# Optimization experiments

Measured on AMD Instinct MI355X. Metric: run time of the kernel, lower is better.

Reference implementation:

```python
import jax, jax.numpy as jnp
import numpy as np

B, N, D = 32, 540, 512
H = 8
DH = D // H
MAX_LEN = 540
POS_CLIP = MAX_LEN - 1


def setup_inputs() -> dict:
    key = jax.random.key(0)
    ks = jax.random.split(key, 12)
    s = 0.02
    inp = {
        "query": jax.random.normal(ks[0], (B, N, D), dtype=jnp.float32),
        "Wq": jax.random.normal(ks[1], (D, D), dtype=jnp.float32) * s,
        "bq": jnp.zeros((D,), jnp.float32),
        "Wk": jax.random.normal(ks[2], (D, D), dtype=jnp.float32) * s,
        "bk": jnp.zeros((D,), jnp.float32),
        "Wv": jax.random.normal(ks[3], (D, D), dtype=jnp.float32) * s,
        "bv": jnp.zeros((D,), jnp.float32),
        "Wh": jax.random.normal(ks[4], (D, D), dtype=jnp.float32) * s,
        "bh": jnp.zeros((D,), jnp.float32),
        "pos_k": jax.random.uniform(ks[5], (2 * POS_CLIP + 1, DH), dtype=jnp.float32, minval=-0.05, maxval=0.05),
        "gamma": jnp.ones((D,), jnp.float32),
        "beta": jnp.zeros((D,), jnp.float32),
        "valid_len": jax.random.randint(ks[6], (B,), 1, N + 1, dtype=jnp.int32),
    }
    return inp


def _split_heads(x):
    # [B, N, D] -> [H*B, N, DH], head-major on axis 0 (matches tf.concat(tf.split(x,H,-1),0))
    return x.reshape(B, N, H, DH).transpose(2, 0, 1, 3).reshape(H * B, N, DH)


def reference(query, Wq, bq, Wk, bk, Wv, bv, Wh, bh, pos_k, gamma, beta, valid_len):
    q = _split_heads(query @ Wq + bq)  # [HB, N, DH]
    k = _split_heads(query @ Wk + bk)
    v = _split_heads(query @ Wv + bv)

    QK = jnp.einsum("xqd,xkd->xqk", q, k)  # [HB, N, N]

    # relative position bias (Shaw et al. 2018)
    rel = jnp.arange(N)[None, :] - jnp.arange(N)[:, None]
    rel = jnp.clip(rel, -POS_CLIP, POS_CLIP) + POS_CLIP
    pos_enc_k = pos_k[rel]  # [N, N, DH]
    QR = jnp.einsum("xqd,qkd->xqk", q, pos_enc_k)

    attn = (QK + QR) / jnp.sqrt(jnp.float32(DH))

    # key-side sequence mask, broadcast over heads and query rows
    key_mask = jnp.arange(N)[None, :] < valid_len[:, None]  # [B, N]
    key_mask = jnp.tile(key_mask[:, None, :], (H, N, 1))  # [HB, N, N]
    attn = jnp.where(key_mask, attn, jnp.float32(-1e12))
    attn = jax.nn.softmax(attn, axis=-1)

    out = jnp.einsum("xqk,xkd->xqd", attn, v)  # [HB, N, DH]
    out = out.reshape(H, B, N, DH).transpose(1, 2, 0, 3).reshape(B, N, D)
    out = out @ Wh + bh
    out = out + query

    # layer norm over last axis
    mean = jnp.mean(out, axis=-1, keepdims=True)
    var = jnp.mean(jnp.square(out - mean), axis=-1, keepdims=True)
    normalized = (out - mean) * jax.lax.rsqrt(var + 1e-7)
    return gamma * normalized + beta
```

## Files before the change

### kernel.cpp

```cpp
#include <hip/hip_runtime.h>
#include <hip/hip_bf16.h>

typedef __hip_bfloat16 bf16;

#define NB 32
#define NSEQ 540
#define ND 512
#define NH 8
#define NDH 64
#define NHB 256
#define NM 17280
#define NPOS 1079
#define VTP 544

typedef __bf16 v8bf __attribute__((ext_vector_type(8)));
typedef float f32x4 __attribute__((ext_vector_type(4)));

union U8 {
  uint4 u;
  unsigned short s[8];
  v8bf v;
};

__device__ __forceinline__ unsigned short f2b(float x) {
  union { float f; unsigned u; } c;
  c.f = x;
  const unsigned r = c.u + 0x7fffu + ((c.u >> 16) & 1u);
  return (unsigned short)(r >> 16);
}

__device__ __forceinline__ float b2f16(unsigned short s) {
  return __uint_as_float(((unsigned)s) << 16);
}

__device__ __forceinline__ void cvt16(const float* __restrict__ p,
                                      unsigned short* __restrict__ dst) {
  unsigned short s[16];
#pragma unroll
  for (int i = 0; i < 4; i++) {
    const float4 v = *(const float4*)(p + i * 4);
    s[i * 4 + 0] = f2b(v.x);
    s[i * 4 + 1] = f2b(v.y);
    s[i * 4 + 2] = f2b(v.z);
    s[i * 4 + 3] = f2b(v.w);
  }
  *(uint4*)dst = *(uint4*)s;
  *(uint4*)(dst + 8) = *(uint4*)(s + 8);
}

__global__ __launch_bounds__(256) void pos_cvt(const float* __restrict__ pos,
                                              unsigned short* __restrict__ posb) {
  const int i = blockIdx.x * 256 + threadIdx.x;
  if (i < NPOS * NDH) posb[i] = f2b(pos[i]);
}

__global__ __launch_bounds__(256) void wcvt(
    const float* __restrict__ Wq, const float* __restrict__ Wk,
    const float* __restrict__ Wv, const float* __restrict__ Wh,
    unsigned short* __restrict__ Wt) {
  __shared__ unsigned short T[64][72];
  const int tid = threadIdx.x;
  const int sel = blockIdx.z;
  const float* W = (sel == 0) ? Wq : (sel == 1) ? Wk : (sel == 2) ? Wv : Wh;
  unsigned short* out = Wt + (size_t)sel * ND * ND;
  const int k0 = blockIdx.x * 64, n0 = blockIdx.y * 64;
  const int r = tid >> 2, g = tid & 3;
  cvt16(W + (size_t)(k0 + r) * ND + n0 + g * 16, &T[r][g * 16]);
  __syncthreads();
  unsigned short s[16];
#pragma unroll
  for (int j = 0; j < 16; j++) s[j] = T[g * 16 + j][r];
  unsigned short* dst = out + (size_t)(n0 + r) * ND + k0 + g * 16;
  *(uint4*)dst = *(uint4*)s;
  *(uint4*)(dst + 8) = *(uint4*)(s + 8);
}

#define GEMM_CORE(APTR)                                                           \
  for (int k0 = 0; k0 < 512; k0 += 32) {                                          \
    __syncthreads();                                                              \
    cvt16(APTR + (size_t)(m0 + srow) * ND + k0 + sh, &As[srow][sh]);              \
    {                                                                             \
      const unsigned short* bp = Bt + (size_t)(n0 + srow) * ND + k0 + sh;         \
      *(uint4*)&Bs[srow][sh] = *(const uint4*)bp;                                 \
      *(uint4*)&Bs[srow][sh + 8] = *(const uint4*)(bp + 8);                       \
    }                                                                             \
    __syncthreads();                                                              \
    U8 af[4], bfr[4];                                                             \
    _Pragma("unroll")                                                             \
    for (int mi = 0; mi < 4; mi++)                                                \
      af[mi].u = *(const uint4*)&As[wr * 64 + mi * 16 + l15][quad * 8];           \
    _Pragma("unroll")                                                             \
    for (int ni = 0; ni < 4; ni++)                                                \
      bfr[ni].u = *(const uint4*)&Bs[wc * 64 + ni * 16 + l15][quad * 8];          \
    _Pragma("unroll")                                                             \
    for (int mi = 0; mi < 4; mi++)                                                \
      _Pragma("unroll")                                                           \
      for (int ni = 0; ni < 4; ni++)                                              \
        acc[mi][ni] = __builtin_amdgcn_mfma_f32_16x16x32_bf16(                    \
            af[mi].v, bfr[ni].v, acc[mi][ni], 0, 0, 0);                           \
  }

__global__ __launch_bounds__(256, 2) void qkv_mfma(
    const float* __restrict__ X, const unsigned short* __restrict__ Wt,
    const float* __restrict__ bq, const float* __restrict__ bk,
    const float* __restrict__ bv,
    bf16* __restrict__ qh, bf16* __restrict__ kh, bf16* __restrict__ vt) {
  __shared__ unsigned short As[128][40];
  __shared__ unsigned short Bs[128][40];
  const int tid = threadIdx.x;
  const int sel = blockIdx.z;
  const unsigned short* Bt = Wt + (size_t)sel * ND * ND;
  const float* bias = (sel == 0) ? bq : (sel == 1) ? bk : bv;
  const int m0 = blockIdx.y * 128, n0 = blockIdx.x * 128;
  const int lane = tid & 63, w = tid >> 6;
  const int wr = w & 1, wc = w >> 1;
  const int l15 = lane & 15, quad = lane >> 4;
  const int srow = tid >> 1, sh = (tid & 1) * 16;

  f32x4 acc[4][4];
#pragma unroll
  for (int mi = 0; mi < 4; mi++)
#pragma unroll
    for (int ni = 0; ni < 4; ni++) acc[mi][ni] = (f32x4){0.f, 0.f, 0.f, 0.f};

  GEMM_CORE(X)

  if (sel != 2) {
    unsigned short* o = (unsigned short*)((sel == 0) ? qh : kh);
#pragma unroll
    for (int mi = 0; mi < 4; mi++) {
      const int m = m0 + wr * 64 + mi * 16 + quad * 4;
      const int bidx = m / NSEQ;
      const int seq0 = m - bidx * NSEQ;
#pragma unroll
      for (int ni = 0; ni < 4; ni++) {
        const int n = n0 + wc * 64 + ni * 16 + l15;
        const int h = n >> 6, dh = n & 63;
        const float bsv = bias[n];
        const size_t base = (((size_t)(h * NB + bidx)) * NSEQ + seq0) * NDH + dh;
#pragma unroll
        for (int i = 0; i < 4; i++)
          o[base + (size_t)i * NDH] = f2b(acc[mi][ni][i] + bsv);
      }
    }
  } else {
    unsigned short* o = (unsigned short*)vt;
#pragma unroll
    for (int mi = 0; mi < 4; mi++) {
      const int m = m0 + wr * 64 + mi * 16 + quad * 4;
      const int bidx = m / NSEQ;
      const int seq0 = m - bidx * NSEQ;
#pragma unroll
      for (int ni = 0; ni < 4; ni++) {
        const int n = n0 + wc * 64 + ni * 16 + l15;
        const int h = n >> 6, dh = n & 63;
        const float bsv = bias[n];
        unsigned short pk[4];
#pragma unroll
        for (int i = 0; i < 4; i++) pk[i] = f2b(acc[mi][ni][i] + bsv);
        *(uint2*)(o + (((size_t)(h * NB + bidx)) * NDH + dh) * VTP + seq0) =
            *(uint2*)pk;
      }
    }
  }
}

__global__ __launch_bounds__(256, 2) void out_mfma(
    const float* __restrict__ ctx, const unsigned short* __restrict__ Wht,
    const float* __restrict__ bh, const float* __restrict__ query,
    float* __restrict__ tmp) {
  __shared__ unsigned short As[128][40];
  __shared__ unsigned short Bs[128][40];
  const int tid = threadIdx.x;
  const unsigned short* Bt = Wht;
  const int m0 = blockIdx.y * 128, n0 = blockIdx.x * 128;
  const int lane = tid & 63, w = tid >> 6;
  const int wr = w & 1, wc = w >> 1;
  const int l15 = lane & 15, quad = lane >> 4;
  const int srow = tid >> 1, sh = (tid & 1) * 16;

  f32x4 acc[4][4];
#pragma unroll
  for (int mi = 0; mi < 4; mi++)
#pragma unroll
    for (int ni = 0; ni < 4; ni++) acc[mi][ni] = (f32x4){0.f, 0.f, 0.f, 0.f};

  GEMM_CORE(ctx)

#pragma unroll
  for (int mi = 0; mi < 4; mi++) {
    const int m = m0 + wr * 64 + mi * 16 + quad * 4;
#pragma unroll
    for (int ni = 0; ni < 4; ni++) {
      const int n = n0 + wc * 64 + ni * 16 + l15;
      const float bsv = bh[n];
#pragma unroll
      for (int i = 0; i < 4; i++) {
        const size_t off = (size_t)(m + i) * ND + n;
        tmp[off] = acc[mi][ni][i] + bsv + query[off];
      }
    }
  }
}

#define PW 584

__global__ __launch_bounds__(256, 5) void attn(
    const bf16* __restrict__ qh, const bf16* __restrict__ kh,
    const bf16* __restrict__ vt, const unsigned short* __restrict__ posb,
    const int* __restrict__ vlen, float* __restrict__ ctx) {
  __shared__ unsigned short P[16][PW];
  __shared__ float Tt[2][16][84];
  __shared__ float red4[16][4];
  __shared__ float sinv[16];

  const int tid = threadIdx.x;
  const int lane = tid & 63;
  const int w = tid >> 6;
  const int l15 = lane & 15;
  const int quad = lane >> 4;
  const int qb = blockIdx.x;
  const int x = blockIdx.y;
  const int b = x & 31, h = x >> 5;
  const int q0 = qb * 16;
  const int valid = vlen[b];
  const int NT = (valid + 63) >> 6;
  const int NC = (valid + 31) >> 5;
  const bf16* qbase = qh + (size_t)x * NSEQ * NDH;
  const unsigned short* kbase = (const unsigned short*)(kh + (size_t)x * NSEQ * NDH);
  const unsigned short* vbase = (const unsigned short*)(vt + (size_t)x * NDH * VTP);

  U8 aq0, aq1;
  {
    const int q = q0 + l15;
    if (q < NSEQ) {
      aq0.u = *(const uint4*)(qbase + (size_t)q * NDH + quad * 8);
      aq1.u = *(const uint4*)(qbase + (size_t)q * NDH + 32 + quad * 8);
    } else {
      aq0.u = make_uint4(0, 0, 0, 0);
      aq1.u = make_uint4(0, 0, 0, 0);
    }
  }

  U8 ck0, ck1, cp0, cp1, ce0, ce1;
  {
    const int key = w * 16 + l15;
    ck0.u = *(const uint4*)(kbase + (size_t)key * NDH + quad * 8);
    ck1.u = *(const uint4*)(kbase + (size_t)key * NDH + 32 + quad * 8);
    const long pr = (long)(524 - q0 + w * 16 + l15);
    cp0.u = *(const uint4*)(posb + pr * NDH + quad * 8);
    cp1.u = *(const uint4*)(posb + pr * NDH + 32 + quad * 8);
    if (w == 0) {
      const long pr2 = (long)(524 - q0 + 64 + l15);
      ce0.u = *(const uint4*)(posb + pr2 * NDH + quad * 8);
      ce1.u = *(const uint4*)(posb + pr2 * NDH + 32 + quad * 8);
    }
  }

  float pmax[4];
#pragma unroll
  for (int i = 0; i < 4; i++) pmax[i] = -1e30f;

  for (int kt = 0; kt < NT; kt++) {
    const int buf = kt & 1;
    U8 nk0, nk1, np0, np1, ne0, ne1;
    if (kt < NT - 1) {
      const int k1 = kt * 64 + 64;
      const int key = k1 + w * 16 + l15;
      nk0.u = *(const uint4*)(kbase + (size_t)key * NDH + quad * 8);
      nk1.u = *(const uint4*)(kbase + (size_t)key * NDH + 32 + quad * 8);
      const long pr = (long)(k1 - q0 + 524 + w * 16 + l15);
      np0.u = *(const uint4*)(posb + pr * NDH + quad * 8);
      np1.u = *(const uint4*)(posb + pr * NDH + 32 + quad * 8);
      if (w == 0) {
        const long pr2 = (long)(k1 - q0 + 524 + 64 + l15);
        ne0.u = *(const uint4*)(posb + pr2 * NDH + quad * 8);
        ne1.u = *(const uint4*)(posb + pr2 * NDH + 32 + quad * 8);
      }
    }

    f32x4 accqk = {0.f, 0.f, 0.f, 0.f};
    accqk = __builtin_amdgcn_mfma_f32_16x16x32_bf16(aq0.v, ck0.v, accqk, 0, 0, 0);
    accqk = __builtin_amdgcn_mfma_f32_16x16x32_bf16(aq1.v, ck1.v, accqk, 0, 0, 0);
    {
      f32x4 accT = {0.f, 0.f, 0.f, 0.f};
      accT = __builtin_amdgcn_mfma_f32_16x16x32_bf16(aq0.v, cp0.v, accT, 0, 0, 0);
      accT = __builtin_amdgcn_mfma_f32_16x16x32_bf16(aq1.v, cp1.v, accT, 0, 0, 0);
#pragma unroll
      for (int i = 0; i < 4; i++) Tt[buf][quad * 4 + i][w * 16 + l15] = accT[i];
      if (w == 0) {
        f32x4 accT2 = {0.f, 0.f, 0.f, 0.f};
        accT2 = __builtin_amdgcn_mfma_f32_16x16x32_bf16(aq0.v, ce0.v, accT2, 0, 0, 0);
        accT2 = __builtin_amdgcn_mfma_f32_16x16x32_bf16(aq1.v, ce1.v, accT2, 0, 0, 0);
#pragma unroll
        for (int i = 0; i < 4; i++) Tt[buf][quad * 4 + i][64 + l15] = accT2[i];
      }
    }
    __syncthreads();
    {
      const int k0 = kt * 64;
      const int kk = w * 16 + l15;
      const bool cm = (k0 + kk) < valid;
#pragma unroll
      for (int i = 0; i < 4; i++) {
        const int qq = quad * 4 + i;
        const float v = (accqk[i] + Tt[buf][qq][kk + 15 - qq]) * 0.125f;
        P[qq][k0 + kk] = f2b(v);
        if (cm) pmax[i] = fmaxf(pmax[i], v);
      }
    }
    ck0 = nk0; ck1 = nk1; cp0 = np0; cp1 = np1;
    if (w == 0) { ce0 = ne0; ce1 = ne1; }
  }

#pragma unroll
  for (int m = 1; m < 16; m <<= 1) {
#pragma unroll
    for (int i = 0; i < 4; i++)
      pmax[i] = fmaxf(pmax[i], __shfl_xor(pmax[i], m, 16));
  }
  if (l15 == 0) {
#pragma unroll
    for (int i = 0; i < 4; i++) red4[quad * 4 + i][w] = pmax[i];
  }

  const int dh = w * 16 + l15;
  const unsigned short* vrow = vbase + (size_t)dh * VTP;
  U8 cv;
  cv.u = *(const uint4*)(vrow + quad * 8);

  __syncthreads();

  {
    const int r = tid >> 4, c = tid & 15;
    const float4 rm = *(const float4*)red4[r];
    const float rowmax = fmaxf(fmaxf(rm.x, rm.y), fmaxf(rm.z, rm.w));
    const int nv = (valid + 7) >> 3;
    float sl = 0.f;
    for (int ch = c; ch < nv; ch += 16) {
      const uint4 u = *(const uint4*)&P[r][ch * 8];
      unsigned ue[4];
#pragma unroll
      for (int jj = 0; jj < 4; jj++) {
        const unsigned uu = ((const unsigned*)&u)[jj];
        const float lo = __uint_as_float(uu << 16);
        const float hi = __uint_as_float(uu & 0xffff0000u);
        float el = __expf(lo - rowmax);
        float eh = __expf(hi - rowmax);
        const int cb = ch * 8 + jj * 2;
        el = (cb < valid) ? el : 0.f;
        eh = (cb + 1 < valid) ? eh : 0.f;
        sl += el + eh;
        ue[jj] = (unsigned)f2b(el) | ((unsigned)f2b(eh) << 16);
      }
      *(uint4*)&P[r][ch * 8] = *(const uint4*)ue;
    }
    for (int ch = c; ch < 72; ch += 16) {
      if (ch >= nv) *(uint4*)&P[r][ch * 8] = make_uint4(0, 0, 0, 0);
    }
#pragma unroll
    for (int m = 1; m < 16; m <<= 1) sl += __shfl_xor(sl, m, 16);
    if (c == 0) sinv[r] = 1.f / sl;
  }
  __syncthreads();

  f32x4 acco = {0.f, 0.f, 0.f, 0.f};
  for (int ci = 0; ci < NC; ci++) {
    U8 nv_;
    if (ci + 1 < NC) nv_.u = *(const uint4*)(vrow + (ci + 1) * 32 + quad * 8);
    U8 ap;
    ap.u = *(const uint4*)&P[l15][ci * 32 + quad * 8];
    acco = __builtin_amdgcn_mfma_f32_16x16x32_bf16(ap.v, cv.v, acco, 0, 0, 0);
    cv = nv_;
  }
#pragma unroll
  for (int i = 0; i < 4; i++) {
    const int q = q0 + quad * 4 + i;
    if (q < NSEQ) {
      ctx[((size_t)b * NSEQ + q) * ND + h * NDH + dh] = acco[i] * sinv[quad * 4 + i];
    }
  }
}

__global__ __launch_bounds__(256) void lnorm(
    const float* __restrict__ tmp, const float* __restrict__ gamma,
    const float* __restrict__ beta, float* __restrict__ out) {
  __shared__ float sred[256];
  const int row = blockIdx.x;
  const int tid = threadIdx.x;
  const size_t base = (size_t)row * 512;
  const float x0 = tmp[base + tid];
  const float x1 = tmp[base + 256 + tid];

  sred[tid] = x0 + x1;
  __syncthreads();
  for (int o = 128; o > 0; o >>= 1) {
    if (tid < o) sred[tid] += sred[tid + o];
    __syncthreads();
  }
  const float mean = sred[0] * (1.f / 512.f);
  __syncthreads();
  const float d0 = x0 - mean, d1 = x1 - mean;
  sred[tid] = d0 * d0 + d1 * d1;
  __syncthreads();
  for (int o = 128; o > 0; o >>= 1) {
    if (tid < o) sred[tid] += sred[tid + o];
    __syncthreads();
  }
  const float var = sred[0] * (1.f / 512.f);
  const float rstd = rsqrtf(var + 1e-7f);
  out[base + tid] = d0 * rstd * gamma[tid] + beta[tid];
  out[base + 256 + tid] = d1 * rstd * gamma[tid + 256] + beta[tid + 256];
}

extern "C" void kernel_launch(void* const* d_in, const int* in_sizes, int n_in,
                              void* d_out, int out_size, void* d_ws, size_t ws_size,
                              hipStream_t stream) {
  const float* query = (const float*)d_in[0];
  const float* Wq = (const float*)d_in[1];
  const float* bq = (const float*)d_in[2];
  const float* Wk = (const float*)d_in[3];
  const float* bk = (const float*)d_in[4];
  const float* Wv = (const float*)d_in[5];
  const float* bv = (const float*)d_in[6];
  const float* Wh = (const float*)d_in[7];
  const float* bh = (const float*)d_in[8];
  const float* pos = (const float*)d_in[9];
  const float* gamma = (const float*)d_in[10];
  const float* beta = (const float*)d_in[11];
  const int* vlen = (const int*)d_in[12];

  bf16* ws = (bf16*)d_ws;
  const size_t QSZ = (size_t)NHB * NSEQ * NDH;
  const size_t VSZ = (size_t)NHB * NDH * VTP;
  bf16* qh = ws;
  bf16* kh = ws + QSZ;
  bf16* vt = ws + 2 * QSZ;
  unsigned short* posb = (unsigned short*)(ws + 2 * QSZ + VSZ);
  unsigned short* Wtb = posb + (size_t)NPOS * NDH;
  float* ctx = (float*)d_out;
  float* tmp = (float*)d_ws;
  (void)ws_size;

  pos_cvt<<<dim3(270), 256, 0, stream>>>(pos, posb);
  wcvt<<<dim3(8, 8, 4), 256, 0, stream>>>(Wq, Wk, Wv, Wh, Wtb);
  qkv_mfma<<<dim3(4, 135, 3), 256, 0, stream>>>(query, Wtb, bq, bk, bv, qh, kh, vt);
  attn<<<dim3(34, 256), 256, 0, stream>>>(qh, kh, vt, posb, vlen, ctx);
  out_mfma<<<dim3(4, 135), 256, 0, stream>>>(ctx, Wtb + 3 * (size_t)ND * ND, bh, query, tmp);
  lnorm<<<NM, 256, 0, stream>>>(tmp, gamma, beta, (float*)d_out);
}
```

Baseline: 345.5 us.

## Replace shared-memory relative-position skew with per-wave shuffles, drop block barrier

The attention loop used to write each wave's Q·pos MFMA tile into a shared buffer, sync the block, and read back diagonally skewed values. Now each wave computes two adjacent 16-row position tiles itself and builds the skew with cross-lane shuffles. This removes the shared-memory round trip and one __syncthreads per key tile, at the cost of doubling the position MFMAs and position loads per wave. The launch-bounds occupancy hint for both GEMM kernels also rises from 2 to 3 blocks per SIMD, which may limit registers.

```diff
diff --git a/kernel.cpp b/kernel.cpp
--- a/kernel.cpp
+++ b/kernel.cpp
@@ -100,7 +100,7 @@
             af[mi].v, bfr[ni].v, acc[mi][ni], 0, 0, 0);                           \
   }
 
-__global__ __launch_bounds__(256, 2) void qkv_mfma(
+__global__ __launch_bounds__(256, 3) void qkv_mfma(
     const float* __restrict__ X, const unsigned short* __restrict__ Wt,
     const float* __restrict__ bq, const float* __restrict__ bk,
     const float* __restrict__ bv,
@@ -165,7 +165,7 @@
   }
 }
 
-__global__ __launch_bounds__(256, 2) void out_mfma(
+__global__ __launch_bounds__(256, 3) void out_mfma(
     const float* __restrict__ ctx, const unsigned short* __restrict__ Wht,
     const float* __restrict__ bh, const float* __restrict__ query,
     float* __restrict__ tmp) {
@@ -210,7 +210,6 @@
     const bf16* __restrict__ vt, const unsigned short* __restrict__ posb,
     const int* __restrict__ vlen, float* __restrict__ ctx) {
   __shared__ unsigned short P[16][PW];
-  __shared__ float Tt[2][16][84];
   __shared__ float red4[16][4];
   __shared__ float sinv[16];
 
@@ -242,7 +241,7 @@
     }
   }
 
-  U8 ck0, ck1, cp0, cp1, ce0, ce1;
+  U8 ck0, ck1, cp0, cp1, cq0, cq1;
   {
     const int key = w * 16 + l15;
     ck0.u = *(const uint4*)(kbase + (size_t)key * NDH + quad * 8);
@@ -250,11 +249,8 @@
     const long pr = (long)(524 - q0 + w * 16 + l15);
     cp0.u = *(const uint4*)(posb + pr * NDH + quad * 8);
     cp1.u = *(const uint4*)(posb + pr * NDH + 32 + quad * 8);
-    if (w == 0) {
-      const long pr2 = (long)(524 - q0 + 64 + l15);
-      ce0.u = *(const uint4*)(posb + pr2 * NDH + quad * 8);
-      ce1.u = *(const uint4*)(posb + pr2 * NDH + 32 + quad * 8);
-    }
+    cq0.u = *(const uint4*)(posb + (pr + 16) * NDH + quad * 8);
+    cq1.u = *(const uint4*)(posb + (pr + 16) * NDH + 32 + quad * 8);
   }
 
   float pmax[4];
@@ -262,8 +258,7 @@
   for (int i = 0; i < 4; i++) pmax[i] = -1e30f;
 
   for (int kt = 0; kt < NT; kt++) {
-    const int buf = kt & 1;
-    U8 nk0, nk1, np0, np1, ne0, ne1;
+    U8 nk0, nk1, np0, np1, nq0, nq1;
     if (kt < NT - 1) {
       const int k1 = kt * 64 + 64;
       const int key = k1 + w * 16 + l15;
@@ -272,31 +267,20 @@
       const long pr = (long)(k1 - q0 + 524 + w * 16 + l15);
       np0.u = *(const uint4*)(posb + pr * NDH + quad * 8);
       np1.u = *(const uint4*)(posb + pr * NDH + 32 + quad * 8);
-      if (w == 0) {
-        const long pr2 = (long)(k1 - q0 + 524 + 64 + l15);
-        ne0.u = *(const uint4*)(posb + pr2 * NDH + quad * 8);
-        ne1.u = *(const uint4*)(posb + pr2 * NDH + 32 + quad * 8);
-      }
+      nq0.u = *(const uint4*)(posb + (pr + 16) * NDH + quad * 8);
+      nq1.u = *(const uint4*)(posb + (pr + 16) * NDH + 32 + quad * 8);
     }
 
     f32x4 accqk = {0.f, 0.f, 0.f, 0.f};
     accqk = __builtin_amdgcn_mfma_f32_16x16x32_bf16(aq0.v, ck0.v, accqk, 0, 0, 0);
     accqk = __builtin_amdgcn_mfma_f32_16x16x32_bf16(aq1.v, ck1.v, accqk, 0, 0, 0);
-    {
-      f32x4 accT = {0.f, 0.f, 0.f, 0.f};
-      accT = __builtin_amdgcn_mfma_f32_16x16x32_bf16(aq0.v, cp0.v, accT, 0, 0, 0);
-      accT = __builtin_amdgcn_mfma_f32_16x16x32_bf16(aq1.v, cp1.v, accT, 0, 0, 0);
-#pragma unroll
-      for (int i = 0; i < 4; i++) Tt[buf][quad * 4 + i][w * 16 + l15] = accT[i];
-      if (w == 0) {
-        f32x4 accT2 = {0.f, 0.f, 0.f, 0.f};
-        accT2 = __builtin_amdgcn_mfma_f32_16x16x32_bf16(aq0.v, ce0.v, accT2, 0, 0, 0);
-        accT2 = __builtin_amdgcn_mfma_f32_16x16x32_bf16(aq1.v, ce1.v, accT2, 0, 0, 0);
-#pragma unroll
-        for (int i = 0; i < 4; i++) Tt[buf][quad * 4 + i][64 + l15] = accT2[i];
-      }
-    }
-    __syncthreads();
+    f32x4 accT0 = {0.f, 0.f, 0.f, 0.f};
+    accT0 = __builtin_amdgcn_mfma_f32_16x16x32_bf16(aq0.v, cp0.v, accT0, 0, 0, 0);
+    accT0 = __builtin_amdgcn_mfma_f32_16x16x32_bf16(aq1.v, cp1.v, accT0, 0, 0, 0);
+    f32x4 accT1 = {0.f, 0.f, 0.f, 0.f};
+    accT1 = __builtin_amdgcn_mfma_f32_16x16x32_bf16(aq0.v, cq0.v, accT1, 0, 0, 0);
+    accT1 = __builtin_amdgcn_mfma_f32_16x16x32_bf16(aq1.v, cq1.v, accT1, 0, 0, 0);
+
     {
       const int k0 = kt * 64;
       const int kk = w * 16 + l15;
@@ -304,13 +288,17 @@
 #pragma unroll
       for (int i = 0; i < 4; i++) {
         const int qq = quad * 4 + i;
-        const float v = (accqk[i] + Tt[buf][qq][kk + 15 - qq]) * 0.125f;
+        const int cr = l15 + 15 - qq;
+        const int src = (quad << 4) | (cr & 15);
+        const float t0 = __shfl(accT0[i], src, 64);
+        const float t1 = __shfl(accT1[i], src, 64);
+        const float tv = (cr < 16) ? t0 : t1;
+        const float v = (accqk[i] + tv) * 0.125f;
         P[qq][k0 + kk] = f2b(v);
         if (cm) pmax[i] = fmaxf(pmax[i], v);
       }
     }
-    ck0 = nk0; ck1 = nk1; cp0 = np0; cp1 = np1;
-    if (w == 0) { ce0 = ne0; ce1 = ne1; }
+    ck0 = nk0; ck1 = nk1; cp0 = np0; cp1 = np1; cq0 = nq0; cq1 = nq1;
   }
 
 #pragma unroll
```

Result: slower. 368.7 us (+6.7%).
